# Performance work log

Hardware: AMD Instinct MI355X
Metric: run time of the kernel (lower is better)

Reference implementation:

```python
import jax, jax.numpy as jnp
import numpy as np

EPS = 1e-5

def convbn_relu(x, W, g, b, m, v):
    # 1x1 conv [O,C] on NCHW input, then inference-mode BN, then ReLU
    y = jnp.einsum('oc,bchw->bohw', W, x)
    scale = (g * jax.lax.rsqrt(v + EPS))[:, None, None]
    y = (y - m[:, None, None]) * scale + b[:, None, None]
    return jax.nn.relu(y)


def setup_inputs() -> dict:
    key = jax.random.key(0)
    ks = jax.random.split(key, 7)
    B, C, H, W = 2, 256, 96, 96
    L = 6  # psi1, psi2, phi1, phi2, f_down, f_up
    x = jax.random.normal(ks[0], (B, C, H, W), dtype=jnp.float32)
    f_k = jax.random.normal(ks[1], (B, C, H, W), dtype=jnp.float32)
    Ws = jax.random.normal(ks[2], (L, C, C), dtype=jnp.float32) * (1.0 / 16.0)
    gammas = jax.random.uniform(ks[3], (L, C), dtype=jnp.float32)
    betas = jax.random.normal(ks[4], (L, C), dtype=jnp.float32) * 0.1
    means = jax.random.normal(ks[5], (L, C), dtype=jnp.float32) * 0.1
    vars_ = jax.random.uniform(ks[6], (L, C), dtype=jnp.float32) + 0.5
    return {"x": x, "f_k": f_k, "Ws": Ws, "gammas": gammas, "betas": betas, "means": means, "vars_": vars_}


def reference(x, f_k, Ws, gammas, betas, means, vars_):
    B, C, H, W = x.shape
    K = Ws.shape[1]
    p = lambda i: (Ws[i], gammas[i], betas[i], means[i], vars_[i])
    # psi(x): two convbn+relu
    q = convbn_relu(convbn_relu(x, *p(0)), *p(1)).reshape(B, K, H * W)
    q = jnp.transpose(q, (0, 2, 1))                      # [B, N, K]
    # phi(f_k): two convbn+relu
    k = convbn_relu(convbn_relu(f_k, *p(2)), *p(3)).reshape(B, K, H * W)  # [B, K, N]
    # f_down(f_k)
    v = convbn_relu(f_k, *p(4)).reshape(B, K, H * W)
    v = jnp.transpose(v, (0, 2, 1))                      # [B, N, K]
    # attention WITHOUT 1/sqrt(d) scaling, as in the original
    sim = jnp.einsum('bnk,bkm->bnm', q, k)               # [B, N, N]
    sim = jax.nn.softmax(sim, axis=-1)
    ctx = jnp.einsum('bnm,bmk->bnk', sim, v)             # [B, N, K]
    ctx = jnp.transpose(ctx, (0, 2, 1)).reshape(B, K, H, W)
    # f_up
    return convbn_relu(ctx, *p(5))
```

## Files before the change

kernel.cpp:

```cpp
#include <hip/hip_runtime.h>
#include <hip/hip_bf16.h>

typedef __bf16 bf16;
typedef __bf16 bf16x8 __attribute__((ext_vector_type(8)));
typedef float floatx4 __attribute__((ext_vector_type(4)));
typedef float floatx16 __attribute__((ext_vector_type(16)));

#define MFMA_BF16(a, b, c) __builtin_amdgcn_mfma_f32_16x16x32_bf16((a), (b), (c), 0, 0, 0)
#define MFMA32(a, b, c) __builtin_amdgcn_mfma_f32_32x32x16_bf16((a), (b), (c), 0, 0, 0)

static constexpr int CH = 256;
static constexpr int NPIX = 9216;
static constexpr int MTOT = 2 * NPIX;
static constexpr int NQB2 = 144;

__device__ __forceinline__ void async16(void* lds, const void* g) {
  __builtin_amdgcn_global_load_lds(
      (const __attribute__((address_space(1))) void*)g,
      (__attribute__((address_space(3))) void*)lds, 16, 0, 0);
}

__device__ __forceinline__ unsigned cvtpk(float lo, float hi) {
  unsigned r;
  asm("v_cvt_pk_bf16_f32 %0, %1, %2" : "=v"(r) : "v"(lo), "v"(hi));
  return r;
}

__device__ __forceinline__ void plswap(unsigned& a, unsigned& b) {
  asm volatile("v_permlane32_swap_b32 %0, %1" : "+v"(a), "+v"(b));
}
__device__ __forceinline__ float xmax32(float v) {
  unsigned a = __builtin_bit_cast(unsigned, v), b = a;
  plswap(a, b);
  return fmaxf(__builtin_bit_cast(float, a), __builtin_bit_cast(float, b));
}
__device__ __forceinline__ float xsum32(float v) {
  unsigned a = __builtin_bit_cast(unsigned, v), b = a;
  plswap(a, b);
  return __builtin_bit_cast(float, a) + __builtin_bit_cast(float, b);
}

__global__ void prep_weights(const float* __restrict__ W,
                             const float* __restrict__ g, const float* __restrict__ b,
                             const float* __restrict__ m, const float* __restrict__ v,
                             bf16* __restrict__ Wh, bf16* __restrict__ Wl,
                             float* __restrict__ scale, float* __restrict__ bias) {
  int i = blockIdx.x * 256 + threadIdx.x;
  if (i < 6 * CH * CH) {
    float w = W[i];
    bf16 h = (bf16)w;
    Wh[i] = h;
    Wl[i] = (bf16)(w - (float)h);
  }
  if (i < 6 * CH) {
    float s = g[i] * rsqrtf(v[i] + 1e-5f);
    scale[i] = s;
    bias[i] = b[i] - m[i] * s;
  }
}

__global__ void split_transpose2(const float* __restrict__ xin, const float* __restrict__ fkin,
                                 bf16* __restrict__ ohx, bf16* __restrict__ olx,
                                 bf16* __restrict__ ohf, bf16* __restrict__ olf) {
  __shared__ float t[64][65];
  int bid = blockIdx.x;
  const float* in; bf16 *oh, *ol;
  if (bid >= 1152) { in = fkin; oh = ohf; ol = olf; bid -= 1152; }
  else             { in = xin;  oh = ohx; ol = olx; }
  int b = bid / 576, rem = bid % 576;
  int ct = rem / 144, nt = rem % 144;
  int c0 = ct * 64, n0 = nt * 64;
  int tid = threadIdx.x;
  int cr = tid >> 4, nc = (tid & 15) * 4;
  for (int rr = 0; rr < 64; rr += 16) {
    int c = cr + rr;
    const float* p = in + ((size_t)(b * CH + c0 + c) * NPIX) + n0 + nc;
    float4 val = *(const float4*)p;
    t[c][nc + 0] = val.x; t[c][nc + 1] = val.y;
    t[c][nc + 2] = val.z; t[c][nc + 3] = val.w;
  }
  __syncthreads();
  int n = tid >> 2, cb = (tid & 3) * 16;
  bf16 hb[16], lb[16];
#pragma unroll
  for (int j = 0; j < 16; j++) {
    float xv = t[cb + j][n];
    bf16 h = (bf16)xv;
    hb[j] = h;
    lb[j] = (bf16)(xv - (float)h);
  }
  size_t idx = (size_t)(b * NPIX + n0 + n) * CH + c0 + cb;
  *(bf16x8*)&oh[idx]     = *(bf16x8*)&hb[0];
  *(bf16x8*)&oh[idx + 8] = *(bf16x8*)&hb[8];
  *(bf16x8*)&ol[idx]     = *(bf16x8*)&lb[0];
  *(bf16x8*)&ol[idx + 8] = *(bf16x8*)&lb[8];
}

__global__ void transpose_bf16(const bf16* __restrict__ in, bf16* __restrict__ out) {
  __shared__ bf16 t[64][72];
  int bid = blockIdx.x;
  int b = bid / 576, rem = bid % 576;
  int ct = rem / 144, nt = rem % 144;
  int c0 = ct * 64, n0 = nt * 64;
  int tid = threadIdx.x;
  int nr = tid >> 4, cc = (tid & 15) * 4;
  for (int rr = 0; rr < 64; rr += 16) {
    int n = nr + rr;
    const bf16* p = in + (size_t)(b * NPIX + n0 + n) * CH + c0 + cc;
#pragma unroll
    for (int j = 0; j < 4; j++) t[cc + j][n] = p[j];
  }
  __syncthreads();
  int c = tid >> 2, nb = (tid & 3) * 16;
  bf16 buf[16];
#pragma unroll
  for (int j = 0; j < 16; j++) buf[j] = t[c][nb + j];
  size_t idx = (size_t)(b * CH + c0 + c) * NPIX + n0 + nb;
  *(bf16x8*)&out[idx]     = *(bf16x8*)&buf[0];
  *(bf16x8*)&out[idx + 8] = *(bf16x8*)&buf[8];
}

__global__ void transpose_out(const float* __restrict__ in, float* __restrict__ out) {
  __shared__ float t[64][65];
  int bid = blockIdx.x;
  int b = bid / 576, rem = bid % 576;
  int ct = rem / 144, nt = rem % 144;
  int c0 = ct * 64, n0 = nt * 64;
  int tid = threadIdx.x;
  int nr = tid >> 4, cc = (tid & 15) * 4;
  for (int rr = 0; rr < 64; rr += 16) {
    int n = nr + rr;
    float4 v = *(const float4*)&in[(size_t)(b * NPIX + n0 + n) * CH + c0 + cc];
    t[cc + 0][n] = v.x; t[cc + 1][n] = v.y; t[cc + 2][n] = v.z; t[cc + 3][n] = v.w;
  }
  __syncthreads();
  int c = tid >> 2, nb = (tid & 3) * 16;
#pragma unroll
  for (int k = 0; k < 4; k++) {
    float4 o4 = make_float4(t[c][nb + 4 * k + 0], t[c][nb + 4 * k + 1],
                            t[c][nb + 4 * k + 2], t[c][nb + 4 * k + 3]);
    *(float4*)&out[(size_t)(b * CH + c0 + c) * NPIX + n0 + nb + 4 * k] = o4;
  }
}

struct ConvJob {
  const bf16 *Ah, *Al, *Bh, *Bl;
  const float *scale, *bias;
  bf16 *Yh, *Yl; float *Yf;
  int mode;
};

__global__ __launch_bounds__(256, 3) void conv128(ConvJob j0, ConvJob j1, ConvJob j2) {
  __shared__ bf16 lds[4][8 * 512];
  int jid = blockIdx.x / 288;
  int bid = blockIdx.x % 288;
  ConvJob j = (jid == 0) ? j0 : (jid == 1) ? j1 : j2;

  int tid = threadIdx.x;
  int w = tid >> 6, l = tid & 63;
  int q = l >> 4, c16 = l & 15;
  int m0 = (bid >> 1) * 128;
  int o0 = (bid & 1) * 128;

  const bf16* src = (w == 0) ? j.Ah : (w == 1) ? j.Al : (w == 2) ? j.Bh : j.Bl;
  int rowbase = (w < 2) ? m0 : o0;
  const bf16* gp = src + (size_t)(rowbase + c16) * CH + q * 8;
  bf16* ldst = &lds[w][0];

  const floatx4 zero4 = {0.f, 0.f, 0.f, 0.f};
  floatx4 acc[4][4];
#pragma unroll
  for (int i = 0; i < 4; i++)
#pragma unroll
    for (int jj = 0; jj < 4; jj++) acc[i][jj] = zero4;

  int mo16 = (w & 1) * 4, no16 = (w >> 1) * 4;

  for (int k0 = 0; k0 < CH; k0 += 32) {
#pragma unroll
    for (int f = 0; f < 8; f++)
      async16(ldst + f * 512, gp + (size_t)f * 16 * CH + k0);
    __syncthreads();

    bf16x8 ah[4], al[4], bh[4], bl[4];
#pragma unroll
    for (int i = 0; i < 4; i++) {
      ah[i] = *(const bf16x8*)&lds[0][(mo16 + i) * 512 + l * 8];
      al[i] = *(const bf16x8*)&lds[1][(mo16 + i) * 512 + l * 8];
      bh[i] = *(const bf16x8*)&lds[2][(no16 + i) * 512 + l * 8];
      bl[i] = *(const bf16x8*)&lds[3][(no16 + i) * 512 + l * 8];
    }
#pragma unroll
    for (int i = 0; i < 4; i++)
#pragma unroll
      for (int jj = 0; jj < 4; jj++) {
        acc[i][jj] = MFMA_BF16(ah[i], bh[jj], acc[i][jj]);
        acc[i][jj] = MFMA_BF16(ah[i], bl[jj], acc[i][jj]);
        acc[i][jj] = MFMA_BF16(al[i], bh[jj], acc[i][jj]);
      }
    __syncthreads();
  }

  int mo = (w & 1) * 64, no = (w >> 1) * 64;
  float sc[4], bs[4];
#pragma unroll
  for (int jj = 0; jj < 4; jj++) {
    int o = o0 + no + 16 * jj + c16;
    sc[jj] = j.scale[o];
    bs[jj] = j.bias[o];
  }
#pragma unroll
  for (int i = 0; i < 4; i++) {
    int nrow = m0 + mo + 16 * i + 4 * q;
#pragma unroll
    for (int jj = 0; jj < 4; jj++) {
      int o = o0 + no + 16 * jj + c16;
#pragma unroll
      for (int r = 0; r < 4; r++) {
        float y = acc[i][jj][r] * sc[jj] + bs[jj];
        y = fmaxf(y, 0.f);
        size_t idx = (size_t)(nrow + r) * CH + o;
        if (j.mode == 2) {
          j.Yf[idx] = y;
        } else if (j.mode == 1) {
          j.Yh[idx] = (bf16)y;
        } else {
          bf16 h = (bf16)y;
          j.Yh[idx] = h;
          j.Yl[idx] = (bf16)(y - (float)h);
        }
      }
    }
  }
}

__global__ __launch_bounds__(256, 4) void conv64(
    const bf16* __restrict__ Ah, const bf16* __restrict__ Al,
    const bf16* __restrict__ Bh, const bf16* __restrict__ Bl,
    const float* __restrict__ scale, const float* __restrict__ bias,
    float* __restrict__ Yf) {
  __shared__ bf16 lds[24 * 512];
  int tid = threadIdx.x;
  int w = tid >> 6, l = tid & 63;
  int q = l >> 4, c16 = l & 15;
  int m0 = (blockIdx.x >> 1) * 64;
  int o0 = (blockIdx.x & 1) * 128;

  const floatx4 zero4 = {0.f, 0.f, 0.f, 0.f};
  floatx4 acc[4][2];
#pragma unroll
  for (int i = 0; i < 4; i++) { acc[i][0] = zero4; acc[i][1] = zero4; }

  for (int k0 = 0; k0 < CH; k0 += 32) {
#pragma unroll
    for (int ff = 0; ff < 6; ff++) {
      int f = w * 6 + ff;
      const bf16* src; int rbase, fl;
      if (f < 4)       { src = Ah; rbase = m0; fl = f; }
      else if (f < 8)  { src = Al; rbase = m0; fl = f - 4; }
      else if (f < 16) { src = Bh; rbase = o0; fl = f - 8; }
      else             { src = Bl; rbase = o0; fl = f - 16; }
      async16(&lds[f * 512], src + (size_t)(rbase + fl * 16 + c16) * CH + k0 + q * 8);
    }
    __syncthreads();

    bf16x8 ah[4], al[4], bh[2], bl[2];
#pragma unroll
    for (int i = 0; i < 4; i++) {
      ah[i] = *(const bf16x8*)&lds[(0 + i) * 512 + l * 8];
      al[i] = *(const bf16x8*)&lds[(4 + i) * 512 + l * 8];
    }
#pragma unroll
    for (int n = 0; n < 2; n++) {
      bh[n] = *(const bf16x8*)&lds[(8 + 2 * w + n) * 512 + l * 8];
      bl[n] = *(const bf16x8*)&lds[(16 + 2 * w + n) * 512 + l * 8];
    }
#pragma unroll
    for (int i = 0; i < 4; i++)
#pragma unroll
      for (int n = 0; n < 2; n++) {
        acc[i][n] = MFMA_BF16(ah[i], bh[n], acc[i][n]);
        acc[i][n] = MFMA_BF16(ah[i], bl[n], acc[i][n]);
        acc[i][n] = MFMA_BF16(al[i], bh[n], acc[i][n]);
      }
    __syncthreads();
  }

  float sc[2], bs[2];
#pragma unroll
  for (int n = 0; n < 2; n++) {
    int o = o0 + 32 * w + 16 * n + c16;
    sc[n] = scale[o];
    bs[n] = bias[o];
  }
#pragma unroll
  for (int i = 0; i < 4; i++) {
    int nrow = m0 + 16 * i + 4 * q;
#pragma unroll
    for (int n = 0; n < 2; n++) {
      int o = o0 + 32 * w + 16 * n + c16;
#pragma unroll
      for (int r = 0; r < 4; r++) {
        float y = acc[i][n][r] * sc[n] + bs[n];
        Yf[(size_t)(nrow + r) * CH + o] = fmaxf(y, 0.f);
      }
    }
  }
}

__global__ __launch_bounds__(256, 2) void attn_part(
    const bf16* __restrict__ Q, const bf16* __restrict__ K, const bf16* __restrict__ Vt,
    float* __restrict__ Opart, float* __restrict__ Mpart, float* __restrict__ Lpart,
    int niter) {
  __shared__ bf16 lK[2][16 * 512];
  __shared__ bf16 lV[2][16 * 512];

  int tid = threadIdx.x;
  int w = tid >> 6, l = tid & 63;
  int ql = l & 31, hi = l >> 5;
  int bid = blockIdx.x;
  int qb = bid % NQB2, s = bid / NQB2;
  int b = qb / 72;
  int n0 = (qb % 72) * 128;
  int kv0 = s * niter * 32;
  size_t qkbase = (size_t)b * NPIX * CH;
  size_t vbase  = (size_t)b * CH * NPIX;

  bf16x8 qf[16];
  {
    const bf16* qp = Q + qkbase + (size_t)(n0 + 32 * w + ql) * CH + 8 * hi;
#pragma unroll
    for (int ks = 0; ks < 16; ks++) qf[ks] = *(const bf16x8*)(qp + ks * 16);
  }

  floatx16 oacc[8];
#pragma unroll
  for (int ct = 0; ct < 8; ct++)
#pragma unroll
    for (int r = 0; r < 16; r++) oacc[ct][r] = 0.f;
  float mrow = -1e30f, lrow = 0.f;

  const bf16* gK = K + qkbase + (size_t)kv0 * CH;
  const bf16* gV = Vt + vbase + kv0;

  auto stage = [&](int bi) {
#pragma unroll
    for (int ff = 0; ff < 4; ff++) {
      int f = 4 * w + ff;
      async16(&lK[bi][f * 512], gK + (size_t)ql * CH + f * 16 + 8 * hi);
      async16(&lV[bi][f * 512],
              gV + (size_t)((f >> 1) * 32 + ql) * NPIX + (f & 1) * 16 + 8 * hi);
    }
  };

  stage(0);

  for (int it = 0; it < niter; it++) {
    int cur = it & 1;
    __syncthreads();

    if (it + 1 < niter) {
      gK += 32 * CH; gV += 32;
      stage(cur ^ 1);
    }

    floatx16 sfA, sfB;
#pragma unroll
    for (int r = 0; r < 16; r++) { sfA[r] = 0.f; sfB[r] = 0.f; }
    __builtin_amdgcn_s_setprio(1);
#pragma unroll
    for (int ks = 0; ks < 16; ks += 2) {
      bf16x8 kf0 = *(const bf16x8*)&lK[cur][(ks + 0) * 512 + l * 8];
      bf16x8 kf1 = *(const bf16x8*)&lK[cur][(ks + 1) * 512 + l * 8];
      sfA = MFMA32(kf0, qf[ks + 0], sfA);
      sfB = MFMA32(kf1, qf[ks + 1], sfB);
    }
    __builtin_amdgcn_s_setprio(0);
    float pm = -1e30f;
#pragma unroll
    for (int r = 0; r < 16; r++) {
      float sv = sfA[r] + sfB[r];
      sfA[r] = sv;
      pm = fmaxf(pm, sv);
    }
    pm = xmax32(pm);

    bool need = pm > mrow + 8.f;
    if (__ballot((int)need) != 0ull) {
      float mn = fmaxf(mrow, pm);
      float alpha = __expf(mrow - mn);
      mrow = mn;
      lrow *= alpha;
      float arow[16];
#pragma unroll
      for (int r = 0; r < 16; r++)
        arow[r] = __shfl(alpha, (r & 3) + 8 * (r >> 2) + 4 * hi);
#pragma unroll
      for (int ct = 0; ct < 8; ct++)
#pragma unroll
        for (int r = 0; r < 16; r++) oacc[ct][r] *= arow[r];
    }

    float p[16];
    float rs = 0.f;
#pragma unroll
    for (int r = 0; r < 16; r++) {
      p[r] = __expf(sfA[r] - mrow);
      rs += p[r];
    }
    lrow += xsum32(rs);

    unsigned pk0 = cvtpk(p[0], p[1]),   pk1 = cvtpk(p[2], p[3]);
    unsigned pk2 = cvtpk(p[4], p[5]),   pk3 = cvtpk(p[6], p[7]);
    unsigned pk4 = cvtpk(p[8], p[9]),   pk5 = cvtpk(p[10], p[11]);
    unsigned pk6 = cvtpk(p[12], p[13]), pk7 = cvtpk(p[14], p[15]);
    plswap(pk0, pk2); plswap(pk1, pk3);
    plswap(pk4, pk6); plswap(pk5, pk7);
    uint4 u0, u1;
    u0.x = pk0; u0.y = pk1; u0.z = pk2; u0.w = pk3;
    u1.x = pk4; u1.y = pk5; u1.z = pk6; u1.w = pk7;
    bf16x8 pa0 = __builtin_bit_cast(bf16x8, u0);
    bf16x8 pa1 = __builtin_bit_cast(bf16x8, u1);

    __builtin_amdgcn_s_setprio(1);
#pragma unroll
    for (int ct = 0; ct < 8; ct++) {
      bf16x8 vb0 = *(const bf16x8*)&lV[cur][(2 * ct + 0) * 512 + l * 8];
      bf16x8 vb1 = *(const bf16x8*)&lV[cur][(2 * ct + 1) * 512 + l * 8];
      oacc[ct] = MFMA32(pa0, vb0, oacc[ct]);
      oacc[ct] = MFMA32(pa1, vb1, oacc[ct]);
    }
    __builtin_amdgcn_s_setprio(0);
  }

  if (hi == 0) {
    Mpart[(size_t)bid * 128 + 32 * w + ql] = mrow;
    Lpart[(size_t)bid * 128 + 32 * w + ql] = lrow;
  }
  float* Ob = Opart + (size_t)bid * 128 * CH;
#pragma unroll
  for (int ct = 0; ct < 8; ct++)
#pragma unroll
    for (int r = 0; r < 16; r++) {
      int row = 32 * w + (r & 3) + 8 * (r >> 2) + 4 * hi;
      Ob[(size_t)row * CH + 32 * ct + ql] = oacc[ct][r];
    }
}

__global__ __launch_bounds__(256) void attn_combine(
    const float* __restrict__ Opart, const float* __restrict__ Mpart,
    const float* __restrict__ Lpart,
    bf16* __restrict__ Oh, bf16* __restrict__ Ol, int S) {
  __shared__ float wgt[8][32];
  __shared__ float invl[32];
  int qb = blockIdx.x >> 2;
  int r0 = (blockIdx.x & 3) * 32;
  int t = threadIdx.x;
  if (t < 32) {
    int row = r0 + t;
    float m = -1e30f;
    for (int s = 0; s < S; s++)
      m = fmaxf(m, Mpart[(size_t)(s * NQB2 + qb) * 128 + row]);
    float lsum = 0.f;
    for (int s = 0; s < S; s++) {
      float wv = __expf(Mpart[(size_t)(s * NQB2 + qb) * 128 + row] - m);
      wgt[s][t] = wv;
      lsum += wv * Lpart[(size_t)(s * NQB2 + qb) * 128 + row];
    }
    invl[t] = 1.0f / lsum;
  }
  __syncthreads();
  int c = t;
  for (int rr = 0; rr < 32; rr++) {
    int row = r0 + rr;
    float acc = 0.f;
    for (int s = 0; s < S; s++)
      acc += wgt[s][rr] * Opart[((size_t)(s * NQB2 + qb) * 128 + row) * CH + c];
    float y = acc * invl[rr];
    size_t idx = (size_t)(qb * 128 + row) * CH + c;
    bf16 h = (bf16)y;
    Oh[idx] = h;
    Ol[idx] = (bf16)(y - (float)h);
  }
}

extern "C" void kernel_launch(void* const* d_in, const int* in_sizes, int n_in,
                              void* d_out, int out_size, void* d_ws, size_t ws_size,
                              hipStream_t stream) {
  const float* x  = (const float*)d_in[0];
  const float* fk = (const float*)d_in[1];
  const float* Ws = (const float*)d_in[2];
  const float* g  = (const float*)d_in[3];
  const float* be = (const float*)d_in[4];
  const float* me = (const float*)d_in[5];
  const float* va = (const float*)d_in[6];
  float* out = (float*)d_out;

  char* p = (char*)d_ws;
  bf16* Wh = (bf16*)p; p += (size_t)6 * CH * CH * 2;
  bf16* Wl = (bf16*)p; p += (size_t)6 * CH * CH * 2;
  float* scale = (float*)p; p += (size_t)6 * CH * 4;
  float* bias  = (float*)p; p += (size_t)6 * CH * 4;
  size_t plane = (size_t)MTOT * CH * 2;
  bf16* S0h = (bf16*)p; p += plane;
  bf16* S0l = (bf16*)p; p += plane;
  bf16* Qh  = (bf16*)p; p += plane;
  bf16* Kh  = (bf16*)p; p += plane;
  bf16* Vh  = (bf16*)p; p += plane;
  bf16* Vt  = (bf16*)p; p += plane;
  char* region = p;

  bf16* S2h = (bf16*)(region);
  bf16* S2l = (bf16*)(region + plane);
  bf16* P1h = (bf16*)(region + 2 * plane);
  bf16* P1l = (bf16*)(region + 3 * plane);
  bf16* F1h = (bf16*)(region + 4 * plane);
  bf16* F1l = (bf16*)(region + 5 * plane);

  size_t base_used = (size_t)(region - (char*)d_ws);
  size_t osz = (size_t)NQB2 * 128 * CH * 4;
  size_t per_split = osz + 2 * (size_t)NQB2 * 128 * 4;
  long avail = (long)ws_size - (long)base_used;
  int S = 1;
  {
    int cand[3] = {3, 2, 1};
    for (int i = 0; i < 3; i++)
      if ((long)cand[i] * (long)per_split <= avail) { S = cand[i]; break; }
  }
  float* Opart = (float*)region;
  float* Mpart = (float*)(region + (size_t)S * osz);
  float* Lpart = Mpart + (size_t)S * NQB2 * 128;
  float* Y5 = (float*)region;

  (void)in_sizes; (void)n_in; (void)out_size;

  prep_weights<<<1536, 256, 0, stream>>>(Ws, g, be, me, va, Wh, Wl, scale, bias);
  split_transpose2<<<2304, 256, 0, stream>>>(x, fk, S0h, S0l, S2h, S2l);

  auto W = [&](int layer) { return Wh + (size_t)layer * CH * CH; };
  auto Wlo = [&](int layer) { return Wl + (size_t)layer * CH * CH; };

  ConvJob psi1  {S0h, S0l, W(0), Wlo(0), scale + 0 * CH, bias + 0 * CH, P1h, P1l, nullptr, 0};
  ConvJob phi1  {S2h, S2l, W(2), Wlo(2), scale + 2 * CH, bias + 2 * CH, F1h, F1l, nullptr, 0};
  ConvJob fdown {S2h, S2l, W(4), Wlo(4), scale + 4 * CH, bias + 4 * CH, Vh, nullptr, nullptr, 1};
  ConvJob psi2  {P1h, P1l, W(1), Wlo(1), scale + 1 * CH, bias + 1 * CH, Qh, nullptr, nullptr, 1};
  ConvJob phi2  {F1h, F1l, W(3), Wlo(3), scale + 3 * CH, bias + 3 * CH, Kh, nullptr, nullptr, 1};

  conv128<<<864, 256, 0, stream>>>(psi1, phi1, fdown);
  conv128<<<576, 256, 0, stream>>>(psi2, phi2, phi2);
  transpose_bf16<<<1152, 256, 0, stream>>>(Vh, Vt);
  attn_part<<<NQB2 * S, 256, 0, stream>>>(Qh, Kh, Vt, Opart, Mpart, Lpart, 288 / S);
  attn_combine<<<NQB2 * 4, 256, 0, stream>>>(Opart, Mpart, Lpart, S0h, S0l, S);
  conv64<<<576, 256, 0, stream>>>(S0h, S0l, W(5), Wlo(5), scale + 5 * CH, bias + 5 * CH, Y5);
  transpose_out<<<1152, 256, 0, stream>>>(Y5, out);
}
```

Before: 483.4 us.

## Fuse V and output transposes into conv epilogues via LDS staging

The f_down conv epilogue and the final conv64 epilogue now stage results in shared memory and write them directly in channel-major layout. This removes the separate transpose_bf16 and transpose_out kernels along with their intermediate buffers and extra global round-trips. In exchange the epilogues gain extra barriers and LDS traffic, and the conv tiles must not straddle the batch boundary.

```diff
diff --git a/kernel.cpp b/kernel.cpp
--- a/kernel.cpp
+++ b/kernel.cpp
@@ -96,53 +96,6 @@
   *(bf16x8*)&ol[idx + 8] = *(bf16x8*)&lb[8];
 }
 
-__global__ void transpose_bf16(const bf16* __restrict__ in, bf16* __restrict__ out) {
-  __shared__ bf16 t[64][72];
-  int bid = blockIdx.x;
-  int b = bid / 576, rem = bid % 576;
-  int ct = rem / 144, nt = rem % 144;
-  int c0 = ct * 64, n0 = nt * 64;
-  int tid = threadIdx.x;
-  int nr = tid >> 4, cc = (tid & 15) * 4;
-  for (int rr = 0; rr < 64; rr += 16) {
-    int n = nr + rr;
-    const bf16* p = in + (size_t)(b * NPIX + n0 + n) * CH + c0 + cc;
-#pragma unroll
-    for (int j = 0; j < 4; j++) t[cc + j][n] = p[j];
-  }
-  __syncthreads();
-  int c = tid >> 2, nb = (tid & 3) * 16;
-  bf16 buf[16];
-#pragma unroll
-  for (int j = 0; j < 16; j++) buf[j] = t[c][nb + j];
-  size_t idx = (size_t)(b * CH + c0 + c) * NPIX + n0 + nb;
-  *(bf16x8*)&out[idx]     = *(bf16x8*)&buf[0];
-  *(bf16x8*)&out[idx + 8] = *(bf16x8*)&buf[8];
-}
-
-__global__ void transpose_out(const float* __restrict__ in, float* __restrict__ out) {
-  __shared__ float t[64][65];
-  int bid = blockIdx.x;
-  int b = bid / 576, rem = bid % 576;
-  int ct = rem / 144, nt = rem % 144;
-  int c0 = ct * 64, n0 = nt * 64;
-  int tid = threadIdx.x;
-  int nr = tid >> 4, cc = (tid & 15) * 4;
-  for (int rr = 0; rr < 64; rr += 16) {
-    int n = nr + rr;
-    float4 v = *(const float4*)&in[(size_t)(b * NPIX + n0 + n) * CH + c0 + cc];
-    t[cc + 0][n] = v.x; t[cc + 1][n] = v.y; t[cc + 2][n] = v.z; t[cc + 3][n] = v.w;
-  }
-  __syncthreads();
-  int c = tid >> 2, nb = (tid & 3) * 16;
-#pragma unroll
-  for (int k = 0; k < 4; k++) {
-    float4 o4 = make_float4(t[c][nb + 4 * k + 0], t[c][nb + 4 * k + 1],
-                            t[c][nb + 4 * k + 2], t[c][nb + 4 * k + 3]);
-    *(float4*)&out[(size_t)(b * CH + c0 + c) * NPIX + n0 + nb + 4 * k] = o4;
-  }
-}
-
 struct ConvJob {
   const bf16 *Ah, *Al, *Bh, *Bl;
   const float *scale, *bias;
@@ -209,6 +162,38 @@
     sc[jj] = j.scale[o];
     bs[jj] = j.bias[o];
   }
+
+  if (j.mode == 3) {
+    bf16* tile = &lds[0][0];
+    int b2 = (m0 >= NPIX) ? 1 : 0;
+    int nr0 = m0 - b2 * NPIX;
+#pragma unroll
+    for (int hc = 0; hc < 2; hc++) {
+      __syncthreads();
+      if ((w >> 1) == hc) {
+#pragma unroll
+        for (int i = 0; i < 4; i++)
+#pragma unroll
+          for (int jj = 0; jj < 4; jj++)
+#pragma unroll
+            for (int r = 0; r < 4; r++) {
+              float y = acc[i][jj][r] * sc[jj] + bs[jj];
+              y = fmaxf(y, 0.f);
+              int chl = no + 16 * jj + c16 - hc * 64;
+              int rowl = mo + 16 * i + 4 * q + r;
+              tile[chl * 136 + rowl] = (bf16)y;
+            }
+      }
+      __syncthreads();
+      int chl = tid >> 2, rseg = (tid & 3) * 32;
+      bf16* dst = j.Yh + ((size_t)(b2 * CH + o0 + hc * 64 + chl)) * NPIX + nr0 + rseg;
+#pragma unroll
+      for (int k = 0; k < 4; k++)
+        *(bf16x8*)(dst + 8 * k) = *(bf16x8*)&tile[chl * 136 + rseg + 8 * k];
+    }
+    return;
+  }
+
 #pragma unroll
   for (int i = 0; i < 4; i++) {
     int nrow = m0 + mo + 16 * i + 4 * q;
@@ -293,18 +278,33 @@
     sc[n] = scale[o];
     bs[n] = bias[o];
   }
-#pragma unroll
-  for (int i = 0; i < 4; i++) {
-    int nrow = m0 + 16 * i + 4 * q;
-#pragma unroll
-    for (int n = 0; n < 2; n++) {
-      int o = o0 + 32 * w + 16 * n + c16;
-#pragma unroll
-      for (int r = 0; r < 4; r++) {
-        float y = acc[i][n][r] * sc[n] + bs[n];
-        Yf[(size_t)(nrow + r) * CH + o] = fmaxf(y, 0.f);
-      }
-    }
+
+  float* tile = (float*)&lds[0];
+  int b2 = (m0 >= NPIX) ? 1 : 0;
+  int nr0 = m0 - b2 * NPIX;
+#pragma unroll
+  for (int hc = 0; hc < 2; hc++) {
+    __syncthreads();
+    if ((w >> 1) == hc) {
+#pragma unroll
+      for (int i = 0; i < 4; i++)
+#pragma unroll
+        for (int n = 0; n < 2; n++)
+#pragma unroll
+          for (int r = 0; r < 4; r++) {
+            float y = acc[i][n][r] * sc[n] + bs[n];
+            y = fmaxf(y, 0.f);
+            int chl = 32 * (w - 2 * hc) + 16 * n + c16;
+            int rowl = 16 * i + 4 * q + r;
+            tile[chl * 68 + rowl] = y;
+          }
+    }
+    __syncthreads();
+    int chl = tid >> 2, rseg = (tid & 3) * 16;
+    float* dst = Yf + ((size_t)(b2 * CH + o0 + hc * 64 + chl)) * NPIX + nr0 + rseg;
+#pragma unroll
+    for (int k = 0; k < 4; k++)
+      *(float4*)(dst + 4 * k) = *(float4*)&tile[chl * 68 + rseg + 4 * k];
   }
 }
 
@@ -506,7 +506,6 @@
   bf16* S0l = (bf16*)p; p += plane;
   bf16* Qh  = (bf16*)p; p += plane;
   bf16* Kh  = (bf16*)p; p += plane;
-  bf16* Vh  = (bf16*)p; p += plane;
   bf16* Vt  = (bf16*)p; p += plane;
   char* region = p;
 
@@ -530,7 +529,6 @@
   float* Opart = (float*)region;
   float* Mpart = (float*)(region + (size_t)S * osz);
   float* Lpart = Mpart + (size_t)S * NQB2 * 128;
-  float* Y5 = (float*)region;
 
   (void)in_sizes; (void)n_in; (void)out_size;
 
@@ -542,15 +540,13 @@
 
   ConvJob psi1  {S0h, S0l, W(0), Wlo(0), scale + 0 * CH, bias + 0 * CH, P1h, P1l, nullptr, 0};
   ConvJob phi1  {S2h, S2l, W(2), Wlo(2), scale + 2 * CH, bias + 2 * CH, F1h, F1l, nullptr, 0};
-  ConvJob fdown {S2h, S2l, W(4), Wlo(4), scale + 4 * CH, bias + 4 * CH, Vh, nullptr, nullptr, 1};
+  ConvJob fdown {S2h, S2l, W(4), Wlo(4), scale + 4 * CH, bias + 4 * CH, Vt, nullptr, nullptr, 3};
   ConvJob psi2  {P1h, P1l, W(1), Wlo(1), scale + 1 * CH, bias + 1 * CH, Qh, nullptr, nullptr, 1};
   ConvJob phi2  {F1h, F1l, W(3), Wlo(3), scale + 3 * CH, bias + 3 * CH, Kh, nullptr, nullptr, 1};
 
   conv128<<<864, 256, 0, stream>>>(psi1, phi1, fdown);
   conv128<<<576, 256, 0, stream>>>(psi2, phi2, phi2);
-  transpose_bf16<<<1152, 256, 0, stream>>>(Vh, Vt);
   attn_part<<<NQB2 * S, 256, 0, stream>>>(Qh, Kh, Vt, Opart, Mpart, Lpart, 288 / S);
   attn_combine<<<NQB2 * 4, 256, 0, stream>>>(Opart, Mpart, Lpart, S0h, S0l, S);
-  conv64<<<576, 256, 0, stream>>>(S0h, S0l, W(5), Wlo(5), scale + 5 * CH, bias + 5 * CH, Y5);
-  transpose_out<<<1152, 256, 0, stream>>>(Y5, out);
-}
+  conv64<<<576, 256, 0, stream>>>(S0h, S0l, W(5), Wlo(5), scale + 5 * CH, bias + 5 * CH, out);
+}
```

Result: faster. 466.8 us (-3.4%).
